# Kernel tuning notes

Measured on AMD Instinct MI355X. Metric: run time of the kernel, lower is better.

The kernel has to match this reference:

```python
import jax, jax.numpy as jnp
import numpy as np

CORR_S = 8        # corr_size
IN_EPS = 1e-5     # torch InstanceNorm2d default eps
L2_EPS = 1e-12    # torch F.normalize default eps


def l2_normalize(x):
    # F.normalize(x, p=2, dim=1)
    n = jnp.sqrt(jnp.sum(x * x, axis=1, keepdims=True))
    return x / jnp.maximum(n, L2_EPS)


def instance_norm(x):
    # InstanceNorm2d(affine=False): per-sample, per-channel over H,W; biased var
    m = jnp.mean(x, axis=(2, 3), keepdims=True)
    v = jnp.var(x, axis=(2, 3), keepdims=True)
    return (x - m) * jax.lax.rsqrt(v + IN_EPS)


def setup_inputs() -> dict:
    key = jax.random.key(0)
    ks = jax.random.split(key, 7)
    B, C, H, W = 16, 256, 96, 96
    fc = 64                      # feat_channel
    p = CORR_S * CORR_S          # 64 correlation channels
    x = jax.random.normal(ks[0], (B, C, H, W), jnp.float32)
    # corr_reduce: Conv1x1(p->fc), IN, ReLU, Conv3x3(fc->fc)
    W1 = jax.random.normal(ks[1], (fc, p), jnp.float32) * 0.05
    b1 = jax.random.normal(ks[2], (fc,), jnp.float32) * 0.05
    W2 = jax.random.normal(ks[3], (fc, fc, 3, 3), jnp.float32) * 0.05
    b2 = jax.random.normal(ks[4], (fc,), jnp.float32) * 0.05
    # feat_adapt: Conv1x1(C+fc=320 -> fc), IN, ReLU
    W3 = jax.random.normal(ks[5], (fc, C + fc), jnp.float32) * 0.05
    b3 = jax.random.normal(ks[6], (fc,), jnp.float32) * 0.05
    return {"x": x, "W1": W1, "b1": b1, "W2": W2, "b2": b2, "W3": W3, "b3": b3}


def reference(x, W1, b1, W2, b2, W3, b3):
    B, C, H, W_ = x.shape
    s = CORR_S
    # AdaptiveAvgPool2d((s,s)): H,W divisible by s -> exact window means
    pooled = x.reshape(B, C, s, H // s, s, W_ // s).mean(axis=(3, 5))  # [B,C,s,s]
    ker = l2_normalize(pooled).reshape(B, C, s * s)  # [B,C,p]
    feat = l2_normalize(x)                            # [B,C,H,W]
    # corr_fun: per-sample 1x1 conv == batched contraction over channels
    corr = jnp.einsum('bcp,bchw->bphw', ker, feat)    # [B,p,H,W]
    # corr_reduce
    h = jnp.einsum('op,bphw->bohw', W1, corr) + b1[None, :, None, None]
    h = jax.nn.relu(instance_norm(h))
    h = jax.lax.conv_general_dilated(
        h, W2, window_strides=(1, 1), padding='SAME',
        dimension_numbers=('NCHW', 'OIHW', 'NCHW')) + b2[None, :, None, None]
    # feat_adapt on cat(x, Red_corr)
    new_feat = jnp.concatenate([x, h], axis=1)        # [B,C+fc,H,W]
    out = jnp.einsum('oc,bchw->bohw', W3, new_feat) + b3[None, :, None, None]
    out = jax.nn.relu(instance_norm(out))
    return out
```

## Files before the change

kernel.cpp:

```cpp
#include <hip/hip_runtime.h>

#define BB 16
#define CC 256
#define HW 9216

typedef short bf16x8 __attribute__((ext_vector_type(8)));
typedef float f32x4 __attribute__((ext_vector_type(4)));

__device__ __forceinline__ unsigned short f2bf(float f) {
  unsigned u = __float_as_uint(f);
  return (unsigned short)((u + 0x7FFFu + ((u >> 16) & 1u)) >> 16);
}
__device__ __forceinline__ float bf2f(unsigned short h) {
  return __uint_as_float(((unsigned)h) << 16);
}

__global__ __launch_bounds__(256) void k_pool(const float* __restrict__ x,
                                              float* __restrict__ pooled) {
  int bc = blockIdx.x;
  const float* plane = x + (size_t)bc * HW;
  __shared__ float rowwin[96][8];
  for (int idx = threadIdx.x; idx < 96 * 8; idx += 256) {
    int y = idx >> 3, wx = idx & 7;
    const float* r = plane + y * 96 + wx * 12;
    float s = 0.f;
#pragma unroll
    for (int i = 0; i < 12; ++i) s += r[i];
    rowwin[y][wx] = s;
  }
  __syncthreads();
  if (threadIdx.x < 64) {
    int wy = threadIdx.x >> 3, wx = threadIdx.x & 7;
    float s = 0.f;
#pragma unroll
    for (int i = 0; i < 12; ++i) s += rowwin[wy * 12 + i][wx];
    pooled[(size_t)bc * 64 + threadIdx.x] = s * (1.0f / 144.0f);
  }
}

__global__ __launch_bounds__(256) void k_invn(const float* __restrict__ pooled,
                                              float* __restrict__ invn) {
  int b = blockIdx.x;
  int p = threadIdx.x & 63, cg = threadIdx.x >> 6;
  const float* pb = pooled + (size_t)b * CC * 64;
  float s = 0.f;
  for (int c = cg; c < CC; c += 4) { float v = pb[c * 64 + p]; s += v * v; }
  __shared__ float sm[4][64];
  sm[cg][p] = s;
  __syncthreads();
  if (threadIdx.x < 64) {
    float tot = sm[0][p] + sm[1][p] + sm[2][p] + sm[3][p];
    invn[b * 64 + p] = 1.0f / fmaxf(sqrtf(tot), 1e-12f);
  }
}

__global__ __launch_bounds__(256) void k_M(const float* __restrict__ pooled,
                                           const float* __restrict__ invn,
                                           const float* __restrict__ W1,
                                           unsigned short* __restrict__ Mbf) {
  int c0 = blockIdx.x * 16, b = blockIdx.y, t = threadIdx.x;
  __shared__ float W1s[64][65];
  __shared__ float kers[16][65];
  __shared__ float invs[64];
  if (t < 64) invs[t] = invn[b * 64 + t];
  for (int i = t; i < 4096; i += 256) W1s[i >> 6][i & 63] = W1[i];
  __syncthreads();
  for (int i = t; i < 1024; i += 256) {
    int c = i >> 6, p = i & 63;
    kers[c][p] = pooled[((size_t)b * CC + c0 + c) * 64 + p] * invs[p];
  }
  __syncthreads();
  int c = t & 15, og = t >> 4;
  float s0 = 0.f, s1 = 0.f, s2 = 0.f, s3 = 0.f;
#pragma unroll
  for (int p = 0; p < 64; ++p) {
    float kv = kers[c][p];
    s0 = fmaf(W1s[og * 4 + 0][p], kv, s0);
    s1 = fmaf(W1s[og * 4 + 1][p], kv, s1);
    s2 = fmaf(W1s[og * 4 + 2][p], kv, s2);
    s3 = fmaf(W1s[og * 4 + 3][p], kv, s3);
  }
  unsigned short* Mb = Mbf + (size_t)b * 64 * 256 + c0 + c;
  Mb[(og * 4 + 0) * 256] = f2bf(s0);
  Mb[(og * 4 + 1) * 256] = f2bf(s1);
  Mb[(og * 4 + 2) * 256] = f2bf(s2);
  Mb[(og * 4 + 3) * 256] = f2bf(s3);
}

__global__ void k_prep(const float* __restrict__ W3, unsigned short* __restrict__ W3bf,
                       const float* __restrict__ W2, unsigned short* __restrict__ W2bf,
                       float* __restrict__ statsbuf) {
  int i = blockIdx.x * 256 + threadIdx.x;
  if (i < 64 * 320) W3bf[i] = f2bf(W3[i]);
  if (i < 9 * 64 * 64) {
    int tap = i >> 12, rem = i & 4095;
    int o = rem >> 6, f = rem & 63;
    W2bf[i] = f2bf(W2[(size_t)(o * 64 + f) * 9 + tap]);
  }
  if (i < 4096) statsbuf[i] = 0.f;
}

__global__ __launch_bounds__(256) void k_tg1(
    const float* __restrict__ x,
    const unsigned short* __restrict__ Mbf,
    const unsigned short* __restrict__ W3bf,
    const float* __restrict__ b1,
    unsigned short* __restrict__ hpix,
    float* __restrict__ y0,
    float* __restrict__ stats1) {
  int b = blockIdx.y;
  int px0 = blockIdx.x * 64;
  int t = threadIdx.x;
  int px = t & 63, cg = t >> 6;
  int w = t >> 6, lane = t & 63, l15 = lane & 15, l4 = lane >> 4;
  __shared__ unsigned char sm[32768];
  __shared__ float sq[64];
  if (t < 64) sq[t] = 0.f;
  __syncthreads();
  float part = 0.f;
  const float* xb = x + (size_t)b * CC * HW + px0 + px;
#pragma unroll
  for (int kk = 0; kk < 8; ++kk) {
    int c = cg * 64 + kk * 8;
    float v[8];
#pragma unroll
    for (int j = 0; j < 8; ++j) {
      v[j] = xb[(size_t)(c + j) * HW];
      part += v[j] * v[j];
    }
    uint4 pk;
    pk.x = (unsigned)f2bf(v[0]) | ((unsigned)f2bf(v[1]) << 16);
    pk.y = (unsigned)f2bf(v[2]) | ((unsigned)f2bf(v[3]) << 16);
    pk.z = (unsigned)f2bf(v[4]) | ((unsigned)f2bf(v[5]) << 16);
    pk.w = (unsigned)f2bf(v[6]) | ((unsigned)f2bf(v[7]) << 16);
    int u = cg * 8 + kk;
    *(uint4*)(sm + px * 512 + ((u ^ (px & 31)) << 4)) = pk;
  }
  atomicAdd(&sq[px], part);
  __syncthreads();
  f32x4 acch[4], accy[4];
#pragma unroll
  for (int nf = 0; nf < 4; ++nf) { f32x4 z = {0.f,0.f,0.f,0.f}; acch[nf] = z; accy[nf] = z; }
  const unsigned short* Ma = Mbf + ((size_t)b * 64 + w * 16 + l15) * 256;
  const unsigned short* Wa = W3bf + (size_t)(w * 16 + l15) * 320;
#pragma unroll
  for (int kk = 0; kk < 8; ++kk) {
    bf16x8 am = *(const bf16x8*)(Ma + kk * 32 + l4 * 8);
    bf16x8 aw = *(const bf16x8*)(Wa + kk * 32 + l4 * 8);
    int u = kk * 4 + l4;
#pragma unroll
    for (int nf = 0; nf < 4; ++nf) {
      int p2 = nf * 16 + l15;
      bf16x8 bfr = *(const bf16x8*)(sm + p2 * 512 + ((u ^ (p2 & 31)) << 4));
      acch[nf] = __builtin_amdgcn_mfma_f32_16x16x32_bf16(am, bfr, acch[nf], 0, 0, 0);
      accy[nf] = __builtin_amdgcn_mfma_f32_16x16x32_bf16(aw, bfr, accy[nf], 0, 0, 0);
    }
  }
  float inv[4];
#pragma unroll
  for (int nf = 0; nf < 4; ++nf)
    inv[nf] = 1.0f / fmaxf(sqrtf(sq[nf * 16 + l15]), 1e-12f);
  float b1v[4];
#pragma unroll
  for (int i = 0; i < 4; ++i) b1v[i] = b1[w * 16 + l4 * 4 + i];
  float s_acc[4], ss_acc[4];
#pragma unroll
  for (int i = 0; i < 4; ++i) { s_acc[i] = 0.f; ss_acc[i] = 0.f; }
  __syncthreads();
#pragma unroll
  for (int nf = 0; nf < 4; ++nf) {
    float hv[4];
#pragma unroll
    for (int i = 0; i < 4; ++i) {
      hv[i] = fmaf(acch[nf][i], inv[nf], b1v[i]);
      s_acc[i] += hv[i];
      ss_acc[i] += hv[i] * hv[i];
    }
    uint2 pk;
    pk.x = (unsigned)f2bf(hv[0]) | ((unsigned)f2bf(hv[1]) << 16);
    pk.y = (unsigned)f2bf(hv[2]) | ((unsigned)f2bf(hv[3]) << 16);
    int p2 = nf * 16 + l15;
    int v = w * 4 + l4;
    *(uint2*)(sm + p2 * 128 + ((v ^ ((p2 & 7) << 1)) << 3)) = pk;
#pragma unroll
    for (int i = 0; i < 4; ++i)
      y0[((size_t)(b * 64 + w * 16 + l4 * 4 + i)) * HW + px0 + nf * 16 + l15] = accy[nf][i];
  }
#pragma unroll
  for (int i = 0; i < 4; ++i) {
    float s = s_acc[i], q = ss_acc[i];
#pragma unroll
    for (int m = 1; m < 16; m <<= 1) {
      s += __shfl_xor(s, m);
      q += __shfl_xor(q, m);
    }
    if (l15 == 0) {
      int o = w * 16 + l4 * 4 + i;
      atomicAdd(&stats1[(b * 64 + o) * 2], s);
      atomicAdd(&stats1[(b * 64 + o) * 2 + 1], q);
    }
  }
  __syncthreads();
  uint4* dst = (uint4*)(hpix + ((size_t)b * HW + px0) * 64);
  for (int i = t; i < 512; i += 256) {
    int p = i >> 3, u16 = i & 7;
    dst[i] = *(const uint4*)(sm + p * 128 + ((u16 ^ (p & 7)) << 4));
  }
}

__global__ __launch_bounds__(256) void k_hnorm(
    const unsigned short* __restrict__ hpix,
    const float* __restrict__ stats1,
    unsigned short* __restrict__ hp) {
  int b = blockIdx.y, tile = blockIdx.x, t = threadIdx.x;
  __shared__ float scs[64], shs[64];
  if (t < 64) {
    float S = stats1[(b * 64 + t) * 2], SS = stats1[(b * 64 + t) * 2 + 1];
    float mean = S * (1.0f / (float)HW);
    float var = SS * (1.0f / (float)HW) - mean * mean;
    float rstd = rsqrtf(var + 1e-5f);
    scs[t] = rstd;
    shs[t] = -mean * rstd;
  }
  __syncthreads();
  const uint2* src = (const uint2*)(hpix + ((size_t)b * HW + tile * 64) * 64);
  uint2* dst = (uint2*)(hp + ((size_t)b * (HW + 192) + 96 + tile * 64) * 64);
  for (int i = t; i < 1024; i += 256) {
    int u = i & 15;
    int c0 = u * 4;
    uint2 v = src[i];
    float f0 = fmaxf(0.f, fmaf(bf2f((unsigned short)(v.x & 0xffff)), scs[c0],     shs[c0]));
    float f1 = fmaxf(0.f, fmaf(bf2f((unsigned short)(v.x >> 16)),    scs[c0 + 1], shs[c0 + 1]));
    float f2 = fmaxf(0.f, fmaf(bf2f((unsigned short)(v.y & 0xffff)), scs[c0 + 2], shs[c0 + 2]));
    float f3 = fmaxf(0.f, fmaf(bf2f((unsigned short)(v.y >> 16)),    scs[c0 + 3], shs[c0 + 3]));
    uint2 o;
    o.x = (unsigned)f2bf(f0) | ((unsigned)f2bf(f1) << 16);
    o.y = (unsigned)f2bf(f2) | ((unsigned)f2bf(f3) << 16);
    dst[i] = o;
  }
  if (tile == 0) {
    uint2 z; z.x = 0; z.y = 0;
    uint2* p0 = (uint2*)(hp + (size_t)b * (HW + 192) * 64);
    uint2* p1 = (uint2*)(hp + ((size_t)b * (HW + 192) + 96 + HW) * 64);
    for (int i = t; i < 96 * 16; i += 256) { p0[i] = z; p1[i] = z; }
  }
}

__global__ __launch_bounds__(256) void k_conv9(
    const unsigned short* __restrict__ hp,
    const unsigned short* __restrict__ W2bf,
    const float* __restrict__ b2,
    const float* __restrict__ y0,
    const unsigned short* __restrict__ W3bf,
    const float* __restrict__ b3,
    unsigned short* __restrict__ opre,
    float* __restrict__ stats2) {
  int b = blockIdx.y;
  int t = threadIdx.x;
  int w = t >> 6, lane = t & 63, l15 = lane & 15, l4 = lane >> 4;
  int pxw = blockIdx.x * 128 + w * 32;
  int xs = pxw % 96;
  __shared__ unsigned char tlds[16384];
  __shared__ float sb[128];
  unsigned char* wb = tlds + w * 4096;
  if (t < 128) sb[t] = 0.f;

  const unsigned short* hpb = hp + ((size_t)b * (HW + 192) + 96) * 64;

  f32x4 acc[4][2];
#pragma unroll
  for (int mf = 0; mf < 4; ++mf)
#pragma unroll
    for (int nf = 0; nf < 2; ++nf) { f32x4 z = {0.f,0.f,0.f,0.f}; acc[mf][nf] = z; }
  bf16x8 zerov = {0,0,0,0,0,0,0,0};

#pragma unroll
  for (int dy = 0; dy < 3; ++dy)
#pragma unroll
    for (int dx = 0; dx < 3; ++dx) {
      int tap = dy * 3 + dx;
      int doff = (dy - 1) * 96 + (dx - 1);
#pragma unroll
      for (int kk = 0; kk < 2; ++kk) {
        bf16x8 afr[4];
#pragma unroll
        for (int mf = 0; mf < 4; ++mf)
          afr[mf] = *(const bf16x8*)(W2bf + ((size_t)(tap * 64 + mf * 16 + l15)) * 64 + kk * 32 + l4 * 8);
#pragma unroll
        for (int nf = 0; nf < 2; ++nf) {
          int p = pxw + nf * 16 + l15;
          int t0n = xs + nf * 16 + l15;
          bool z = (dx == 0 && t0n == 0) || (dx == 2 && t0n == 95);
          int pidx = z ? p : (p + doff);
          bf16x8 bfr = *(const bf16x8*)(hpb + (size_t)pidx * 64 + kk * 32 + l4 * 8);
          if (z) bfr = zerov;
#pragma unroll
          for (int mf = 0; mf < 4; ++mf)
            acc[mf][nf] = __builtin_amdgcn_mfma_f32_16x16x32_bf16(afr[mf], bfr, acc[mf][nf], 0, 0, 0);
        }
      }
    }
  float b2v[4][4];
#pragma unroll
  for (int mf = 0; mf < 4; ++mf)
#pragma unroll
    for (int i = 0; i < 4; ++i) b2v[mf][i] = b2[mf * 16 + l4 * 4 + i];
#pragma unroll
  for (int mf = 0; mf < 4; ++mf)
#pragma unroll
    for (int nf = 0; nf < 2; ++nf) {
      int lpx = nf * 16 + l15;
      uint2 pk;
      pk.x = (unsigned)f2bf(acc[mf][nf][0] + b2v[mf][0]) |
             ((unsigned)f2bf(acc[mf][nf][1] + b2v[mf][1]) << 16);
      pk.y = (unsigned)f2bf(acc[mf][nf][2] + b2v[mf][2]) |
             ((unsigned)f2bf(acc[mf][nf][3] + b2v[mf][3]) << 16);
      int v = mf * 4 + l4;
      *(uint2*)(wb + lpx * 128 + ((v ^ ((lpx & 7) << 1)) << 3)) = pk;
    }
  __syncthreads();
  f32x4 acc2[4][2];
#pragma unroll
  for (int mf = 0; mf < 4; ++mf)
#pragma unroll
    for (int i = 0; i < 4; ++i) {
      const float* yr = y0 + ((size_t)(b * 64 + mf * 16 + l4 * 4 + i)) * HW + pxw + l15;
#pragma unroll
      for (int nf = 0; nf < 2; ++nf) acc2[mf][nf][i] = yr[nf * 16];
    }
#pragma unroll
  for (int kk = 0; kk < 2; ++kk) {
    bf16x8 afr[4];
#pragma unroll
    for (int mf = 0; mf < 4; ++mf)
      afr[mf] = *(const bf16x8*)(W3bf + (size_t)(mf * 16 + l15) * 320 + 256 + kk * 32 + l4 * 8);
#pragma unroll
    for (int nf = 0; nf < 2; ++nf) {
      int lpx = nf * 16 + l15;
      int v0 = kk * 8 + l4 * 2;
      union { bf16x8 v; uint2 h[2]; } bb;
      bb.h[0] = *(const uint2*)(wb + lpx * 128 + (((v0    ) ^ ((lpx & 7) << 1)) << 3));
      bb.h[1] = *(const uint2*)(wb + lpx * 128 + (((v0 + 1) ^ ((lpx & 7) << 1)) << 3));
#pragma unroll
      for (int mf = 0; mf < 4; ++mf)
        acc2[mf][nf] = __builtin_amdgcn_mfma_f32_16x16x32_bf16(afr[mf], bb.v, acc2[mf][nf], 0, 0, 0);
    }
  }
  float b3v[4][4];
#pragma unroll
  for (int mf = 0; mf < 4; ++mf)
#pragma unroll
    for (int i = 0; i < 4; ++i) b3v[mf][i] = b3[mf * 16 + l4 * 4 + i];
#pragma unroll
  for (int mf = 0; mf < 4; ++mf)
#pragma unroll
    for (int i = 0; i < 4; ++i) {
      float s = 0.f, q = 0.f;
#pragma unroll
      for (int nf = 0; nf < 2; ++nf) {
        float hv = acc2[mf][nf][i] + b3v[mf][i];
        s += hv;
        q += hv * hv;
      }
#pragma unroll
      for (int m = 1; m < 16; m <<= 1) {
        s += __shfl_xor(s, m);
        q += __shfl_xor(q, m);
      }
      if (l15 == 0) {
        int o = mf * 16 + l4 * 4 + i;
        atomicAdd(&sb[o * 2], s);
        atomicAdd(&sb[o * 2 + 1], q);
      }
    }
  __syncthreads();
  if (t < 64) {
    atomicAdd(&stats2[(b * 64 + t) * 2], sb[t * 2]);
    atomicAdd(&stats2[(b * 64 + t) * 2 + 1], sb[t * 2 + 1]);
  }
#pragma unroll
  for (int mf = 0; mf < 4; ++mf)
#pragma unroll
    for (int nf = 0; nf < 2; ++nf) {
      int p = pxw + nf * 16 + l15;
      uint2 pk;
      pk.x = (unsigned)f2bf(acc2[mf][nf][0] + b3v[mf][0]) |
             ((unsigned)f2bf(acc2[mf][nf][1] + b3v[mf][1]) << 16);
      pk.y = (unsigned)f2bf(acc2[mf][nf][2] + b3v[mf][2]) |
             ((unsigned)f2bf(acc2[mf][nf][3] + b3v[mf][3]) << 16);
      *(uint2*)(opre + ((size_t)b * HW + p) * 64 + mf * 16 + l4 * 4) = pk;
    }
}

__global__ __launch_bounds__(256) void k_apply(const unsigned short* __restrict__ opre,
                                               const float* __restrict__ stats2,
                                               float* __restrict__ out) {
  int b = blockIdx.y, px0 = blockIdx.x * 64, t = threadIdx.x;
  __shared__ float tile[64][68];
  __shared__ float scs[64], shs[64];
  if (t < 64) {
    float S = stats2[(b * 64 + t) * 2], SS = stats2[(b * 64 + t) * 2 + 1];
    float mean = S * (1.0f / (float)HW);
    float var = SS * (1.0f / (float)HW) - mean * mean;
    float rstd = rsqrtf(var + 1e-5f);
    scs[t] = rstd;
    shs[t] = -mean * rstd;
  }
  __syncthreads();
  const unsigned* src = (const unsigned*)(opre + ((size_t)b * HW + px0) * 64);
  for (int i = t; i < 2048; i += 256) {
    int px = i >> 5, q = i & 31;
    unsigned v = src[i];
    int o = q * 2;
    float f0 = bf2f((unsigned short)(v & 0xffff));
    float f1 = bf2f((unsigned short)(v >> 16));
    tile[o][px]     = fmaxf(0.f, fmaf(f0, scs[o], shs[o]));
    tile[o + 1][px] = fmaxf(0.f, fmaf(f1, scs[o + 1], shs[o + 1]));
  }
  __syncthreads();
  for (int j = t; j < 1024; j += 256) {
    int o = j >> 4, w4 = j & 15;
    float4 v = *(const float4*)(&tile[o][w4 * 4]);
    *(float4*)(out + ((size_t)(b * 64) + o) * HW + px0 + w4 * 4) = v;
  }
}

extern "C" void kernel_launch(void* const* d_in, const int* in_sizes, int n_in,
                              void* d_out, int out_size, void* d_ws, size_t ws_size,
                              hipStream_t stream) {
  const float* x  = (const float*)d_in[0];
  const float* W1 = (const float*)d_in[1];
  const float* b1 = (const float*)d_in[2];
  const float* W2 = (const float*)d_in[3];
  const float* b2 = (const float*)d_in[4];
  const float* W3 = (const float*)d_in[5];
  const float* b3 = (const float*)d_in[6];
  float* out = (float*)d_out;

  float* ws = (float*)d_ws;
  float* pooled = ws;
  float* invn   = ws + 262144;
  float* stats  = ws + 263168;
  float* stats1 = stats;
  float* stats2 = stats + 2048;
  unsigned short* Mbf  = (unsigned short*)(ws + 267264);
  unsigned short* W3bf = (unsigned short*)(ws + 398336);
  unsigned short* W2bf = (unsigned short*)(ws + 408576);
  unsigned short* hpix = (unsigned short*)(ws + 427008);
  float* y0            = ws + 5145600;
  unsigned short* opre = (unsigned short*)(ws + 14582784);
  unsigned short* hp   = (unsigned short*)(ws + 19301376);

  k_prep<<<dim3(144), dim3(256), 0, stream>>>(W3, W3bf, W2, W2bf, stats);
  k_pool<<<dim3(BB * CC), dim3(256), 0, stream>>>(x, pooled);
  k_invn<<<dim3(BB), dim3(256), 0, stream>>>(pooled, invn);
  k_M<<<dim3(16, BB), dim3(256), 0, stream>>>(pooled, invn, W1, Mbf);
  k_tg1<<<dim3(144, BB), dim3(256), 0, stream>>>(x, Mbf, W3bf, b1, hpix, y0, stats1);
  k_hnorm<<<dim3(144, BB), dim3(256), 0, stream>>>(hpix, stats1, hp);
  k_conv9<<<dim3(72, BB), dim3(256), 0, stream>>>(hp, W2bf, b2, y0, W3bf, b3, opre, stats2);
  k_apply<<<dim3(144, BB), dim3(256), 0, stream>>>(opre, stats2, out);
}
```

Baseline: 251.6 us.

## Vectorize x loads in tg1 and store y0 as pixel-major bf16

```diff
diff --git a/kernel.cpp b/kernel.cpp
--- a/kernel.cpp
+++ b/kernel.cpp
@@ -106,37 +106,56 @@
     const unsigned short* __restrict__ W3bf,
     const float* __restrict__ b1,
     unsigned short* __restrict__ hpix,
-    float* __restrict__ y0,
+    unsigned short* __restrict__ y0b,
     float* __restrict__ stats1) {
   int b = blockIdx.y;
   int px0 = blockIdx.x * 64;
   int t = threadIdx.x;
-  int px = t & 63, cg = t >> 6;
   int w = t >> 6, lane = t & 63, l15 = lane & 15, l4 = lane >> 4;
+  int cq = lane >> 4, pq = lane & 15;
   __shared__ unsigned char sm[32768];
   __shared__ float sq[64];
   if (t < 64) sq[t] = 0.f;
   __syncthreads();
-  float part = 0.f;
-  const float* xb = x + (size_t)b * CC * HW + px0 + px;
-#pragma unroll
-  for (int kk = 0; kk < 8; ++kk) {
-    int c = cg * 64 + kk * 8;
-    float v[8];
+  float part[4] = {0.f, 0.f, 0.f, 0.f};
+  const float* xb = x + (size_t)b * CC * HW + px0 + pq * 4;
+#pragma unroll
+  for (int half = 0; half < 2; ++half) {
+    float4 vv[8];
 #pragma unroll
     for (int j = 0; j < 8; ++j) {
-      v[j] = xb[(size_t)(c + j) * HW];
-      part += v[j] * v[j];
-    }
-    uint4 pk;
-    pk.x = (unsigned)f2bf(v[0]) | ((unsigned)f2bf(v[1]) << 16);
-    pk.y = (unsigned)f2bf(v[2]) | ((unsigned)f2bf(v[3]) << 16);
-    pk.z = (unsigned)f2bf(v[4]) | ((unsigned)f2bf(v[5]) << 16);
-    pk.w = (unsigned)f2bf(v[6]) | ((unsigned)f2bf(v[7]) << 16);
-    int u = cg * 8 + kk;
-    *(uint4*)(sm + px * 512 + ((u ^ (px & 31)) << 4)) = pk;
-  }
-  atomicAdd(&sq[px], part);
+      int c = w * 64 + cq * 16 + half * 8 + j;
+      vv[j] = *(const float4*)(xb + (size_t)c * HW);
+      part[0] = fmaf(vv[j].x, vv[j].x, part[0]);
+      part[1] = fmaf(vv[j].y, vv[j].y, part[1]);
+      part[2] = fmaf(vv[j].z, vv[j].z, part[2]);
+      part[3] = fmaf(vv[j].w, vv[j].w, part[3]);
+    }
+    int u = w * 8 + cq * 2 + half;
+#pragma unroll
+    for (int j2 = 0; j2 < 4; ++j2) {
+      float e[8];
+#pragma unroll
+      for (int j = 0; j < 8; ++j) {
+        float4 q = vv[j];
+        e[j] = (j2 == 0) ? q.x : (j2 == 1) ? q.y : (j2 == 2) ? q.z : q.w;
+      }
+      uint4 pk;
+      pk.x = (unsigned)f2bf(e[0]) | ((unsigned)f2bf(e[1]) << 16);
+      pk.y = (unsigned)f2bf(e[2]) | ((unsigned)f2bf(e[3]) << 16);
+      pk.z = (unsigned)f2bf(e[4]) | ((unsigned)f2bf(e[5]) << 16);
+      pk.w = (unsigned)f2bf(e[6]) | ((unsigned)f2bf(e[7]) << 16);
+      int px = pq * 4 + j2;
+      *(uint4*)(sm + px * 512 + ((u ^ (px & 31) ^ ((px >> 3) & 7)) << 4)) = pk;
+    }
+  }
+#pragma unroll
+  for (int j2 = 0; j2 < 4; ++j2) {
+    float s = part[j2];
+    s += __shfl_xor(s, 16);
+    s += __shfl_xor(s, 32);
+    if (cq == 0) atomicAdd(&sq[pq * 4 + j2], s);
+  }
   __syncthreads();
   f32x4 acch[4], accy[4];
 #pragma unroll
@@ -151,7 +170,7 @@
 #pragma unroll
     for (int nf = 0; nf < 4; ++nf) {
       int p2 = nf * 16 + l15;
-      bf16x8 bfr = *(const bf16x8*)(sm + p2 * 512 + ((u ^ (p2 & 31)) << 4));
+      bf16x8 bfr = *(const bf16x8*)(sm + p2 * 512 + ((u ^ (p2 & 31) ^ ((p2 >> 3) & 7)) << 4));
       acch[nf] = __builtin_amdgcn_mfma_f32_16x16x32_bf16(am, bfr, acch[nf], 0, 0, 0);
       accy[nf] = __builtin_amdgcn_mfma_f32_16x16x32_bf16(aw, bfr, accy[nf], 0, 0, 0);
     }
@@ -176,15 +195,16 @@
       s_acc[i] += hv[i];
       ss_acc[i] += hv[i] * hv[i];
     }
+    int p2 = nf * 16 + l15;
+    int v = w * 4 + l4;
     uint2 pk;
     pk.x = (unsigned)f2bf(hv[0]) | ((unsigned)f2bf(hv[1]) << 16);
     pk.y = (unsigned)f2bf(hv[2]) | ((unsigned)f2bf(hv[3]) << 16);
-    int p2 = nf * 16 + l15;
-    int v = w * 4 + l4;
     *(uint2*)(sm + p2 * 128 + ((v ^ ((p2 & 7) << 1)) << 3)) = pk;
-#pragma unroll
-    for (int i = 0; i < 4; ++i)
-      y0[((size_t)(b * 64 + w * 16 + l4 * 4 + i)) * HW + px0 + nf * 16 + l15] = accy[nf][i];
+    uint2 pky;
+    pky.x = (unsigned)f2bf(accy[nf][0]) | ((unsigned)f2bf(accy[nf][1]) << 16);
+    pky.y = (unsigned)f2bf(accy[nf][2]) | ((unsigned)f2bf(accy[nf][3]) << 16);
+    *(uint2*)(sm + 16384 + p2 * 128 + ((v ^ ((p2 & 7) << 1)) << 3)) = pky;
   }
 #pragma unroll
   for (int i = 0; i < 4; ++i) {
@@ -201,10 +221,12 @@
     }
   }
   __syncthreads();
-  uint4* dst = (uint4*)(hpix + ((size_t)b * HW + px0) * 64);
+  uint4* dsth = (uint4*)(hpix + ((size_t)b * HW + px0) * 64);
+  uint4* dsty = (uint4*)(y0b + ((size_t)b * HW + px0) * 64);
   for (int i = t; i < 512; i += 256) {
     int p = i >> 3, u16 = i & 7;
-    dst[i] = *(const uint4*)(sm + p * 128 + ((u16 ^ (p & 7)) << 4));
+    dsth[i] = *(const uint4*)(sm + p * 128 + ((u16 ^ (p & 7)) << 4));
+    dsty[i] = *(const uint4*)(sm + 16384 + p * 128 + ((u16 ^ (p & 7)) << 4));
   }
 }
 
@@ -250,7 +272,7 @@
     const unsigned short* __restrict__ hp,
     const unsigned short* __restrict__ W2bf,
     const float* __restrict__ b2,
-    const float* __restrict__ y0,
+    const unsigned short* __restrict__ y0b,
     const unsigned short* __restrict__ W3bf,
     const float* __restrict__ b3,
     unsigned short* __restrict__ opre,
@@ -320,13 +342,16 @@
     }
   __syncthreads();
   f32x4 acc2[4][2];
-#pragma unroll
-  for (int mf = 0; mf < 4; ++mf)
-#pragma unroll
-    for (int i = 0; i < 4; ++i) {
-      const float* yr = y0 + ((size_t)(b * 64 + mf * 16 + l4 * 4 + i)) * HW + pxw + l15;
-#pragma unroll
-      for (int nf = 0; nf < 2; ++nf) acc2[mf][nf][i] = yr[nf * 16];
+  const unsigned short* yb = y0b + ((size_t)b * HW + pxw) * 64;
+#pragma unroll
+  for (int mf = 0; mf < 4; ++mf)
+#pragma unroll
+    for (int nf = 0; nf < 2; ++nf) {
+      uint2 v = *(const uint2*)(yb + (size_t)(nf * 16 + l15) * 64 + mf * 16 + l4 * 4);
+      acc2[mf][nf][0] = bf2f((unsigned short)(v.x & 0xffff));
+      acc2[mf][nf][1] = bf2f((unsigned short)(v.x >> 16));
+      acc2[mf][nf][2] = bf2f((unsigned short)(v.y & 0xffff));
+      acc2[mf][nf][3] = bf2f((unsigned short)(v.y >> 16));
     }
 #pragma unroll
   for (int kk = 0; kk < 2; ++kk) {
@@ -447,7 +472,7 @@
   unsigned short* W3bf = (unsigned short*)(ws + 398336);
   unsigned short* W2bf = (unsigned short*)(ws + 408576);
   unsigned short* hpix = (unsigned short*)(ws + 427008);
-  float* y0            = ws + 5145600;
+  unsigned short* y0b  = (unsigned short*)(ws + 5145600);
   unsigned short* opre = (unsigned short*)(ws + 14582784);
   unsigned short* hp   = (unsigned short*)(ws + 19301376);
 
@@ -455,8 +480,8 @@
   k_pool<<<dim3(BB * CC), dim3(256), 0, stream>>>(x, pooled);
   k_invn<<<dim3(BB), dim3(256), 0, stream>>>(pooled, invn);
   k_M<<<dim3(16, BB), dim3(256), 0, stream>>>(pooled, invn, W1, Mbf);
-  k_tg1<<<dim3(144, BB), dim3(256), 0, stream>>>(x, Mbf, W3bf, b1, hpix, y0, stats1);
+  k_tg1<<<dim3(144, BB), dim3(256), 0, stream>>>(x, Mbf, W3bf, b1, hpix, y0b, stats1);
   k_hnorm<<<dim3(144, BB), dim3(256), 0, stream>>>(hpix, stats1, hp);
-  k_conv9<<<dim3(72, BB), dim3(256), 0, stream>>>(hp, W2bf, b2, y0, W3bf, b3, opre, stats2);
+  k_conv9<<<dim3(72, BB), dim3(256), 0, stream>>>(hp, W2bf, b2, y0b, W3bf, b3, opre, stats2);
   k_apply<<<dim3(144, BB), dim3(256), 0, stream>>>(opre, stats2, out);
 }
```

Result: slower. 265.6 us (+5.6%).

## Store y0 intermediate as pixel-major bf16 and halve k_tg1 shared memory

Applied to the files above, without the earlier changes.

```diff
diff --git a/kernel.cpp b/kernel.cpp
--- a/kernel.cpp
+++ b/kernel.cpp
@@ -100,61 +100,68 @@
   if (i < 4096) statsbuf[i] = 0.f;
 }
 
-__global__ __launch_bounds__(256) void k_tg1(
+__global__ __launch_bounds__(256, 8) void k_tg1(
     const float* __restrict__ x,
     const unsigned short* __restrict__ Mbf,
     const unsigned short* __restrict__ W3bf,
     const float* __restrict__ b1,
     unsigned short* __restrict__ hpix,
-    float* __restrict__ y0,
+    unsigned short* __restrict__ y0b,
     float* __restrict__ stats1) {
   int b = blockIdx.y;
   int px0 = blockIdx.x * 64;
   int t = threadIdx.x;
   int px = t & 63, cg = t >> 6;
   int w = t >> 6, lane = t & 63, l15 = lane & 15, l4 = lane >> 4;
-  __shared__ unsigned char sm[32768];
+  __shared__ unsigned char sm[16384];
   __shared__ float sq[64];
   if (t < 64) sq[t] = 0.f;
   __syncthreads();
-  float part = 0.f;
+
   const float* xb = x + (size_t)b * CC * HW + px0 + px;
-#pragma unroll
-  for (int kk = 0; kk < 8; ++kk) {
-    int c = cg * 64 + kk * 8;
-    float v[8];
-#pragma unroll
-    for (int j = 0; j < 8; ++j) {
-      v[j] = xb[(size_t)(c + j) * HW];
-      part += v[j] * v[j];
-    }
-    uint4 pk;
-    pk.x = (unsigned)f2bf(v[0]) | ((unsigned)f2bf(v[1]) << 16);
-    pk.y = (unsigned)f2bf(v[2]) | ((unsigned)f2bf(v[3]) << 16);
-    pk.z = (unsigned)f2bf(v[4]) | ((unsigned)f2bf(v[5]) << 16);
-    pk.w = (unsigned)f2bf(v[6]) | ((unsigned)f2bf(v[7]) << 16);
-    int u = cg * 8 + kk;
-    *(uint4*)(sm + px * 512 + ((u ^ (px & 31)) << 4)) = pk;
-  }
-  atomicAdd(&sq[px], part);
-  __syncthreads();
-  f32x4 acch[4], accy[4];
-#pragma unroll
-  for (int nf = 0; nf < 4; ++nf) { f32x4 z = {0.f,0.f,0.f,0.f}; acch[nf] = z; accy[nf] = z; }
   const unsigned short* Ma = Mbf + ((size_t)b * 64 + w * 16 + l15) * 256;
   const unsigned short* Wa = W3bf + (size_t)(w * 16 + l15) * 320;
-#pragma unroll
-  for (int kk = 0; kk < 8; ++kk) {
-    bf16x8 am = *(const bf16x8*)(Ma + kk * 32 + l4 * 8);
-    bf16x8 aw = *(const bf16x8*)(Wa + kk * 32 + l4 * 8);
-    int u = kk * 4 + l4;
-#pragma unroll
-    for (int nf = 0; nf < 4; ++nf) {
-      int p2 = nf * 16 + l15;
-      bf16x8 bfr = *(const bf16x8*)(sm + p2 * 512 + ((u ^ (p2 & 31)) << 4));
-      acch[nf] = __builtin_amdgcn_mfma_f32_16x16x32_bf16(am, bfr, acch[nf], 0, 0, 0);
-      accy[nf] = __builtin_amdgcn_mfma_f32_16x16x32_bf16(aw, bfr, accy[nf], 0, 0, 0);
-    }
+
+  f32x4 acch[4], accy[4];
+#pragma unroll
+  for (int nf = 0; nf < 4; ++nf) { f32x4 z = {0.f,0.f,0.f,0.f}; acch[nf] = z; accy[nf] = z; }
+  float part = 0.f;
+
+#pragma unroll
+  for (int r = 0; r < 2; ++r) {
+#pragma unroll
+    for (int kk = 0; kk < 4; ++kk) {
+      int c = r * 128 + cg * 32 + kk * 8;
+      float v[8];
+#pragma unroll
+      for (int j = 0; j < 8; ++j) {
+        v[j] = xb[(size_t)(c + j) * HW];
+        part += v[j] * v[j];
+      }
+      uint4 pk;
+      pk.x = (unsigned)f2bf(v[0]) | ((unsigned)f2bf(v[1]) << 16);
+      pk.y = (unsigned)f2bf(v[2]) | ((unsigned)f2bf(v[3]) << 16);
+      pk.z = (unsigned)f2bf(v[4]) | ((unsigned)f2bf(v[5]) << 16);
+      pk.w = (unsigned)f2bf(v[6]) | ((unsigned)f2bf(v[7]) << 16);
+      int u = cg * 4 + kk;
+      *(uint4*)(sm + px * 256 + ((u ^ (px & 15)) << 4)) = pk;
+    }
+    if (r == 1) atomicAdd(&sq[px], part);
+    __syncthreads();
+#pragma unroll
+    for (int kk = 0; kk < 4; ++kk) {
+      bf16x8 am = *(const bf16x8*)(Ma + r * 128 + kk * 32 + l4 * 8);
+      bf16x8 aw = *(const bf16x8*)(Wa + r * 128 + kk * 32 + l4 * 8);
+      int u = kk * 4 + l4;
+#pragma unroll
+      for (int nf = 0; nf < 4; ++nf) {
+        int p2 = nf * 16 + l15;
+        bf16x8 bfr = *(const bf16x8*)(sm + p2 * 256 + ((u ^ (p2 & 15)) << 4));
+        acch[nf] = __builtin_amdgcn_mfma_f32_16x16x32_bf16(am, bfr, acch[nf], 0, 0, 0);
+        accy[nf] = __builtin_amdgcn_mfma_f32_16x16x32_bf16(aw, bfr, accy[nf], 0, 0, 0);
+      }
+    }
+    __syncthreads();
   }
   float inv[4];
 #pragma unroll
@@ -166,7 +173,6 @@
   float s_acc[4], ss_acc[4];
 #pragma unroll
   for (int i = 0; i < 4; ++i) { s_acc[i] = 0.f; ss_acc[i] = 0.f; }
-  __syncthreads();
 #pragma unroll
   for (int nf = 0; nf < 4; ++nf) {
     float hv[4];
@@ -176,15 +182,16 @@
       s_acc[i] += hv[i];
       ss_acc[i] += hv[i] * hv[i];
     }
+    int p2 = nf * 16 + l15;
+    int v = w * 4 + l4;
     uint2 pk;
     pk.x = (unsigned)f2bf(hv[0]) | ((unsigned)f2bf(hv[1]) << 16);
     pk.y = (unsigned)f2bf(hv[2]) | ((unsigned)f2bf(hv[3]) << 16);
-    int p2 = nf * 16 + l15;
-    int v = w * 4 + l4;
     *(uint2*)(sm + p2 * 128 + ((v ^ ((p2 & 7) << 1)) << 3)) = pk;
-#pragma unroll
-    for (int i = 0; i < 4; ++i)
-      y0[((size_t)(b * 64 + w * 16 + l4 * 4 + i)) * HW + px0 + nf * 16 + l15] = accy[nf][i];
+    uint2 pky;
+    pky.x = (unsigned)f2bf(accy[nf][0]) | ((unsigned)f2bf(accy[nf][1]) << 16);
+    pky.y = (unsigned)f2bf(accy[nf][2]) | ((unsigned)f2bf(accy[nf][3]) << 16);
+    *(uint2*)(sm + 8192 + p2 * 128 + ((v ^ ((p2 & 7) << 1)) << 3)) = pky;
   }
 #pragma unroll
   for (int i = 0; i < 4; ++i) {
@@ -201,10 +208,12 @@
     }
   }
   __syncthreads();
-  uint4* dst = (uint4*)(hpix + ((size_t)b * HW + px0) * 64);
+  uint4* dsth = (uint4*)(hpix + ((size_t)b * HW + px0) * 64);
+  uint4* dsty = (uint4*)(y0b + ((size_t)b * HW + px0) * 64);
   for (int i = t; i < 512; i += 256) {
     int p = i >> 3, u16 = i & 7;
-    dst[i] = *(const uint4*)(sm + p * 128 + ((u16 ^ (p & 7)) << 4));
+    dsth[i] = *(const uint4*)(sm + p * 128 + ((u16 ^ (p & 7)) << 4));
+    dsty[i] = *(const uint4*)(sm + 8192 + p * 128 + ((u16 ^ (p & 7)) << 4));
   }
 }
 
@@ -250,7 +259,7 @@
     const unsigned short* __restrict__ hp,
     const unsigned short* __restrict__ W2bf,
     const float* __restrict__ b2,
-    const float* __restrict__ y0,
+    const unsigned short* __restrict__ y0b,
     const unsigned short* __restrict__ W3bf,
     const float* __restrict__ b3,
     unsigned short* __restrict__ opre,
@@ -320,13 +329,16 @@
     }
   __syncthreads();
   f32x4 acc2[4][2];
-#pragma unroll
-  for (int mf = 0; mf < 4; ++mf)
-#pragma unroll
-    for (int i = 0; i < 4; ++i) {
-      const float* yr = y0 + ((size_t)(b * 64 + mf * 16 + l4 * 4 + i)) * HW + pxw + l15;
-#pragma unroll
-      for (int nf = 0; nf < 2; ++nf) acc2[mf][nf][i] = yr[nf * 16];
+  const unsigned short* yb = y0b + ((size_t)b * HW + pxw) * 64;
+#pragma unroll
+  for (int mf = 0; mf < 4; ++mf)
+#pragma unroll
+    for (int nf = 0; nf < 2; ++nf) {
+      uint2 v = *(const uint2*)(yb + (size_t)(nf * 16 + l15) * 64 + mf * 16 + l4 * 4);
+      acc2[mf][nf][0] = bf2f((unsigned short)(v.x & 0xffff));
+      acc2[mf][nf][1] = bf2f((unsigned short)(v.x >> 16));
+      acc2[mf][nf][2] = bf2f((unsigned short)(v.y & 0xffff));
+      acc2[mf][nf][3] = bf2f((unsigned short)(v.y >> 16));
     }
 #pragma unroll
   for (int kk = 0; kk < 2; ++kk) {
@@ -447,7 +459,7 @@
   unsigned short* W3bf = (unsigned short*)(ws + 398336);
   unsigned short* W2bf = (unsigned short*)(ws + 408576);
   unsigned short* hpix = (unsigned short*)(ws + 427008);
-  float* y0            = ws + 5145600;
+  unsigned short* y0b  = (unsigned short*)(ws + 5145600);
   unsigned short* opre = (unsigned short*)(ws + 14582784);
   unsigned short* hp   = (unsigned short*)(ws + 19301376);
 
@@ -455,8 +467,8 @@
   k_pool<<<dim3(BB * CC), dim3(256), 0, stream>>>(x, pooled);
   k_invn<<<dim3(BB), dim3(256), 0, stream>>>(pooled, invn);
   k_M<<<dim3(16, BB), dim3(256), 0, stream>>>(pooled, invn, W1, Mbf);
-  k_tg1<<<dim3(144, BB), dim3(256), 0, stream>>>(x, Mbf, W3bf, b1, hpix, y0, stats1);
+  k_tg1<<<dim3(144, BB), dim3(256), 0, stream>>>(x, Mbf, W3bf, b1, hpix, y0b, stats1);
   k_hnorm<<<dim3(144, BB), dim3(256), 0, stream>>>(hpix, stats1, hp);
-  k_conv9<<<dim3(72, BB), dim3(256), 0, stream>>>(hp, W2bf, b2, y0, W3bf, b3, opre, stats2);
+  k_conv9<<<dim3(72, BB), dim3(256), 0, stream>>>(hp, W2bf, b2, y0b, W3bf, b3, opre, stats2);
   k_apply<<<dim3(144, BB), dim3(256), 0, stream>>>(opre, stats2, out);
 }
```

Result: slower. 320.4 us (+27.4%).
